# Kernel tuning notes

Measured on AMD Instinct MI355X. Metric: run time of the kernel, lower is better.

The kernel has to match this reference:

```python
import jax, jax.numpy as jnp
import numpy as np

B, T, N, D, H, C = 32, 64, 22, 512, 8, 128
DEPTH = D // H


def setup_inputs() -> dict:
    key = jax.random.key(0)
    ks = jax.random.split(key, 10)
    s = 0.02
    return {
        "x": jax.random.normal(ks[0], (B, T, N, D), jnp.float32),
        "context": jax.random.normal(ks[1], (B, C, D), jnp.float32),
        "Wq": jax.random.normal(ks[2], (N, D, D), jnp.float32) * s,  # per-joint Q proj
        "bq": jax.random.normal(ks[3], (N, D), jnp.float32) * s,
        "Wk": jax.random.normal(ks[4], (D, D), jnp.float32) * s,
        "bk": jax.random.normal(ks[5], (D,), jnp.float32) * s,
        "Wv": jax.random.normal(ks[6], (D, D), jnp.float32) * s,
        "bv": jax.random.normal(ks[7], (D,), jnp.float32) * s,
        "Wout": jax.random.normal(ks[8], (D, D), jnp.float32) * s,
        "bout": jax.random.normal(ks[9], (D,), jnp.float32) * s,
    }


def reference(x, context, Wq, bq, Wk, bk, Wv, bv, Wout, bout):
    b, t, n, d = x.shape
    c = context.shape[1]
    h, dh = H, DEPTH
    # Per-joint Q projection fused into one batched GEMM: [B,T,N,D] x [N,D,D] -> [B,T,N,D]
    q = jnp.einsum('btnd,ndf->btnf', x, Wq) + bq  # bq broadcasts over (B,T)
    # Shared K/V computed ONCE (original recomputes per joint; math identical)
    k = context @ Wk + bk  # [B,C,D]
    v = context @ Wv + bv  # [B,C,D]
    # Split heads
    qh = q.reshape(b, t, n, h, dh)
    kh = k.reshape(b, c, h, dh)
    vh = v.reshape(b, c, h, dh)
    scale = 1.0 / float(np.sqrt(dh))
    # Attention logits per joint: [B,N,H,T,C]
    logits = jnp.einsum('btnhd,bchd->bnhtc', qh, kh) * scale
    attn = jax.nn.softmax(logits, axis=-1)
    # Attend shared V, merge heads: [B,T,N,D]
    o = jnp.einsum('bnhtc,bchd->btnhd', attn, vh).reshape(b, t, n, d)
    # Shared output projection
    return o @ Wout + bout
```

## Files before the change

### kernel.cpp

```cpp
#include <hip/hip_runtime.h>
#include <hip/hip_bf16.h>

#define NB 32
#define NT 64
#define NJ 22
#define ND 512
#define NH 8
#define NC 128
#define NDH 64
#define NR 1408

typedef __attribute__((ext_vector_type(8))) short s16x8;
typedef __attribute__((ext_vector_type(4))) float fx4;

static __device__ __forceinline__ unsigned short f2bf(float f) {
    unsigned u = __builtin_bit_cast(unsigned, f);
    u += 0x7fffu + ((u >> 16) & 1u);
    return (unsigned short)(u >> 16);
}

static __device__ __forceinline__ fx4 mfma16(s16x8 a, s16x8 b, fx4 c) {
    return __builtin_amdgcn_mfma_f32_16x16x32_bf16(a, b, c, 0, 0, 0);
}

static __device__ __forceinline__ void gload16(const void* g, void* l) {
    __builtin_amdgcn_global_load_lds(
        (const __attribute__((address_space(1))) void*)g,
        (__attribute__((address_space(3))) void*)l,
        16, 0, 0);
}

template <int DIV>
__global__ __launch_bounds__(256) void convswz_k(const float* __restrict__ src,
                                                 unsigned short* __restrict__ dst)
{
    const long i = ((long)blockIdx.x * 256 + threadIdx.x) * 8;
    const unsigned row = (unsigned)(i >> 9);
    const int  key = (int)((row / (unsigned)DIV) & 7u);
    const int  c   = (int)((i >> 3) & 7);
    const int  cs  = c ^ key;
    const long j   = (i & ~63L) | ((long)cs << 3);
    const float4 a = *reinterpret_cast<const float4*>(src + i);
    const float4 b = *reinterpret_cast<const float4*>(src + i + 4);
    unsigned short t[8];
    t[0]=f2bf(a.x); t[1]=f2bf(a.y); t[2]=f2bf(a.z); t[3]=f2bf(a.w);
    t[4]=f2bf(b.x); t[5]=f2bf(b.y); t[6]=f2bf(b.z); t[7]=f2bf(b.w);
    *reinterpret_cast<s16x8*>(dst + j) = *reinterpret_cast<s16x8*>(t);
}

__global__ __launch_bounds__(256) void twconv_k(const float* __restrict__ W,
                                                unsigned short* __restrict__ Wt,
                                                long zsrc, long zdst)
{
    __shared__ float T[64][65];
    const int tid = threadIdx.x;
    W  += blockIdx.z * zsrc + (long)blockIdx.x * 64 * 512 + blockIdx.y * 64;
    Wt += blockIdx.z * zdst + (long)blockIdx.y * 64 * 512 + blockIdx.x * 64;
    const int r = tid >> 2, c0 = (tid & 3) * 16;
    #pragma unroll
    for (int i = 0; i < 4; ++i) {
        const float4 p = *reinterpret_cast<const float4*>(W + (long)r * 512 + c0 + i*4);
        T[r][c0 + i*4 + 0] = p.x; T[r][c0 + i*4 + 1] = p.y;
        T[r][c0 + i*4 + 2] = p.z; T[r][c0 + i*4 + 3] = p.w;
    }
    __syncthreads();
    unsigned short o[16];
    #pragma unroll
    for (int i = 0; i < 16; ++i) o[i] = f2bf(T[c0 + i][r]);
    const int ch0 = ((c0 >> 3) ^ (r & 7));
    *reinterpret_cast<s16x8*>(Wt + (long)r * 512 + ch0*8)       = *reinterpret_cast<s16x8*>(o);
    *reinterpret_cast<s16x8*>(Wt + (long)r * 512 + (ch0^1)*8)   = *reinterpret_cast<s16x8*>(o + 8);
}

template <typename TC, int MODE>
__global__ __launch_bounds__(256) void gemm128_k(
    const unsigned short* __restrict__ A, long lda,
    const unsigned short* __restrict__ Bt,
    const float* __restrict__ bias,
    TC* __restrict__ C, long ldc,
    long jsA, long jsW, long jsB, long jsC)
{
    __shared__ unsigned short As[2][128*64];
    __shared__ unsigned short Bs[2][128*64];

    const int tid = threadIdx.x;
    const int w = tid >> 6, lane = tid & 63;
    const long j = blockIdx.z;

    const int nx = gridDim.x;
    const int nwg = nx * gridDim.y;
    int lin = blockIdx.y * nx + blockIdx.x;
    lin = (lin & 7) * (nwg >> 3) + (lin >> 3);
    const int bx = lin % nx, by = lin / nx;

    A    += (long)bx * 128 * lda + j * jsA;
    Bt   += j * jsW + (long)by * 128 * 512;
    bias += j * jsB + by * 128;
    if constexpr (MODE == 0)
        C += (long)bx * 128 * ldc + j * jsC + by * 128;

    const int srow = lane >> 3;
    const int scol = (lane & 7) * 8;
    const unsigned short* Ag = A  + (long)(w*8 + srow) * lda + scol;
    const unsigned short* Bg = Bt + (long)(w*8 + srow) * 512 + scol;

    const int lr = lane & 15, lk = lane >> 4;
    const int wm = w >> 1, wn = w & 1;

    fx4 acc[4][4] = {};

    auto STAGE = [&](int buf, int kt) {
        char* Al = (char*)&As[buf][0] + w * 1024;
        char* Bl = (char*)&Bs[buf][0] + w * 1024;
        #pragma unroll
        for (int it = 0; it < 4; ++it)
            gload16(Ag + (long)it * 32 * lda + kt, Al + it * 4096);
        #pragma unroll
        for (int it = 0; it < 4; ++it)
            gload16(Bg + (long)it * 32 * 512 + kt, Bl + it * 4096);
    };

    auto COMPUTE = [&](int buf) {
        #pragma unroll
        for (int ks = 0; ks < 2; ++ks) {
            const int cha = (ks*4 + lk) ^ (lr & 7);
            s16x8 a[4], b[4];
            #pragma unroll
            for (int m = 0; m < 4; ++m)
                a[m] = *reinterpret_cast<const s16x8*>(&As[buf][(wm*64 + m*16 + lr)*64 + cha*8]);
            #pragma unroll
            for (int n = 0; n < 4; ++n)
                b[n] = *reinterpret_cast<const s16x8*>(&Bs[buf][(wn*64 + n*16 + lr)*64 + cha*8]);
            #pragma unroll
            for (int m = 0; m < 4; ++m)
                #pragma unroll
                for (int n = 0; n < 4; ++n)
                    acc[m][n] = mfma16(a[m], b[n], acc[m][n]);
        }
    };

    STAGE(0, 0);
    __syncthreads();
    #pragma unroll
    for (int t = 0; t < 7; ++t) {
        const int cur = t & 1;
        STAGE(cur ^ 1, (t + 1) * 64);
        COMPUTE(cur);
        __syncthreads();
    }
    COMPUTE(1);

    #pragma unroll
    for (int n = 0; n < 4; ++n) {
        const int col = wn*64 + n*16 + lr;
        const float bv = bias[col];
        #pragma unroll
        for (int m = 0; m < 4; ++m) {
            #pragma unroll
            for (int r = 0; r < 4; ++r) {
                const int row = wm*64 + m*16 + lk*4 + r;
                const float val = acc[m][n][r] + bv;
                if constexpr (MODE == 0) {
                    if constexpr (sizeof(TC) == 2)
                        reinterpret_cast<unsigned short*>(C)[(long)row*ldc + col] = f2bf(val);
                    else
                        reinterpret_cast<float*>(C)[(long)row*ldc + col] = val;
                } else {
                    const int grow = bx*128 + row;
                    const int gcol = by*128 + col;
                    const int b = grow >> 7, c = grow & 127;
                    const int hh = gcol >> 6, dh = gcol & 63;
                    unsigned short* Cp = reinterpret_cast<unsigned short*>(C);
                    if constexpr (MODE == 1) {
                        const int dhs = (dh & 7) | ((((dh >> 3) ^ (c & 7)) & 7) << 3);
                        Cp[(((long)b*8 + hh)*128 + c)*64 + dhs] = f2bf(val);
                    } else {
                        const int cs = (c & 7) | ((((c >> 3) ^ (dh & 7)) & 15) << 3);
                        Cp[(((long)b*8 + hh)*64 + dh)*128 + cs] = f2bf(val);
                    }
                }
            }
        }
    }
}

__global__ __launch_bounds__(256) void attn2_k(
    const unsigned short* __restrict__ q,
    const unsigned short* __restrict__ kt,
    const unsigned short* __restrict__ vt,
    unsigned short* __restrict__ o)
{
    __shared__ unsigned short Ps[128*136];
    __shared__ unsigned short Ks[128*64];
    __shared__ unsigned short Vs[64*128];

    const int tid = threadIdx.x;
    const int w = tid >> 6, lane = tid & 63;
    const int lr = lane & 15, lk = lane >> 4;
    const int r0 = blockIdx.x * 128;
    const int h = blockIdx.y;
    const int b = blockIdx.z;

    const unsigned short* qg = q + ((long)b*NR + r0 + w*32 + (lane>>3))*512
                                 + h*64 + (lane & 7)*8;
    const unsigned short* kg = kt + ((long)(b*8+h))*8192 + (w*4)*512 + lane*8;
    const unsigned short* vg = vt + ((long)(b*8+h))*8192 + (w*4)*512 + lane*8;

    #pragma unroll
    for (int it = 0; it < 4; ++it) {
        gload16(qg + (long)it*8*512, (char*)Ps + (w*32 + it*8)*128);
        gload16(kg + it*512, (char*)Ks + (w*4 + it)*1024);
        gload16(vg + it*512, (char*)Vs + (w*4 + it)*1024);
    }
    __syncthreads();

    s16x8 aq[2][2];
    #pragma unroll
    for (int m = 0; m < 2; ++m)
        #pragma unroll
        for (int kk = 0; kk < 2; ++kk)
            aq[m][kk] = *reinterpret_cast<const s16x8*>(
                &Ps[(w*32 + m*16 + lr)*64 + kk*32 + lk*8]);
    __syncthreads();

    fx4 s[2][8] = {};
    #pragma unroll
    for (int kk = 0; kk < 2; ++kk) {
        #pragma unroll
        for (int f = 0; f < 8; ++f) {
            const int c = f*16 + lr;
            const int chunk = (kk*4 + lk) ^ (c & 7);
            s16x8 bk = *reinterpret_cast<const s16x8*>(&Ks[c*64 + chunk*8]);
            s[0][f] = mfma16(aq[0][kk], bk, s[0][f]);
            s[1][f] = mfma16(aq[1][kk], bk, s[1][f]);
        }
    }

    const float SC = 0.125f * 1.44269504088896340736f;
    #pragma unroll
    for (int m = 0; m < 2; ++m) {
        #pragma unroll
        for (int r = 0; r < 4; ++r) {
            float mx = -3.0e38f;
            #pragma unroll
            for (int f = 0; f < 8; ++f) mx = fmaxf(mx, s[m][f][r]);
            #pragma unroll
            for (int off = 1; off < 16; off <<= 1) mx = fmaxf(mx, __shfl_xor(mx, off));
            float p[8]; float sum = 0.f;
            #pragma unroll
            for (int f = 0; f < 8; ++f) {
                p[f] = exp2f((s[m][f][r] - mx) * SC);
                sum += p[f];
            }
            #pragma unroll
            for (int off = 1; off < 16; off <<= 1) sum += __shfl_xor(sum, off);
            const float inv = 1.0f / sum;
            const int row = w*32 + m*16 + lk*4 + r;
            #pragma unroll
            for (int f = 0; f < 8; ++f)
                Ps[row*136 + f*16 + lr] = f2bf(p[f] * inv);
        }
    }

    fx4 oacc[2][4] = {};
    #pragma unroll
    for (int kt4 = 0; kt4 < 4; ++kt4) {
        s16x8 ap[2];
        #pragma unroll
        for (int m = 0; m < 2; ++m)
            ap[m] = *reinterpret_cast<const s16x8*>(
                &Ps[(w*32 + m*16 + lr)*136 + kt4*32 + lk*8]);
        #pragma unroll
        for (int bn = 0; bn < 4; ++bn) {
            const int dh = bn*16 + lr;
            const int chunk = (kt4*4 + lk) ^ (dh & 7);
            s16x8 bv = *reinterpret_cast<const s16x8*>(&Vs[dh*128 + chunk*8]);
            oacc[0][bn] = mfma16(ap[0], bv, oacc[0][bn]);
            oacc[1][bn] = mfma16(ap[1], bv, oacc[1][bn]);
        }
    }

    unsigned short* ob = o + ((long)b*NR + r0)*512 + h*64;
    #pragma unroll
    for (int m = 0; m < 2; ++m)
        #pragma unroll
        for (int bn = 0; bn < 4; ++bn)
            #pragma unroll
            for (int r = 0; r < 4; ++r) {
                const int row = w*32 + m*16 + lk*4 + r;
                const int colg = bn*16 + lr;
                const int ch = ((colg >> 3) ^ (row & 7));
                ob[(long)row*512 + ch*8 + (lr & 7)] = f2bf(oacc[m][bn][r]);
            }
}

extern "C" void kernel_launch(void* const* d_in, const int* in_sizes, int n_in,
                              void* d_out, int out_size, void* d_ws, size_t ws_size,
                              hipStream_t stream)
{
    const float* x    = (const float*)d_in[0];
    const float* ctx  = (const float*)d_in[1];
    const float* Wq   = (const float*)d_in[2];
    const float* bq   = (const float*)d_in[3];
    const float* Wk   = (const float*)d_in[4];
    const float* bk   = (const float*)d_in[5];
    const float* Wv   = (const float*)d_in[6];
    const float* bv   = (const float*)d_in[7];
    const float* Wout = (const float*)d_in[8];
    const float* bout = (const float*)d_in[9];
    float* out = (float*)d_out;

    const size_t NX  = (size_t)45056 * 512;
    const size_t NKV = (size_t)4096 * 512;
    const size_t NW  = (size_t)512 * 512;

    unsigned short* xbf   = (unsigned short*)d_ws;
    unsigned short* qbf   = xbf   + NX;
    unsigned short* cbf   = qbf   + NX;
    unsigned short* ktp   = cbf   + NKV;
    unsigned short* vtp   = ktp   + NKV;
    unsigned short* WqT   = vtp   + NKV;
    unsigned short* WkT   = WqT   + 22 * NW;
    unsigned short* WvT   = WkT   + NW;
    unsigned short* WoutT = WvT   + NW;
    unsigned short* obf   = xbf;

    convswz_k<NJ><<<dim3(NX / 2048), 256, 0, stream>>>(x, xbf);
    convswz_k<1><<<dim3(NKV / 2048), 256, 0, stream>>>(ctx, cbf);
    twconv_k<<<dim3(8, 8, 22), 256, 0, stream>>>(Wq,   WqT,   (long)NW, (long)NW);
    twconv_k<<<dim3(8, 8, 1),  256, 0, stream>>>(Wk,   WkT,   0, 0);
    twconv_k<<<dim3(8, 8, 1),  256, 0, stream>>>(Wv,   WvT,   0, 0);
    twconv_k<<<dim3(8, 8, 1),  256, 0, stream>>>(Wout, WoutT, 0, 0);

    gemm128_k<unsigned short, 0><<<dim3(16, 4, NJ), 256, 0, stream>>>(
        xbf, (long)NJ*ND, WqT, bq, qbf, (long)NJ*ND,
        (long)ND, (long)NW, (long)ND, (long)ND);

    gemm128_k<unsigned short, 1><<<dim3(32, 4, 1), 256, 0, stream>>>(
        cbf, ND, WkT, bk, ktp, ND, 0, 0, 0, 0);
    gemm128_k<unsigned short, 2><<<dim3(32, 4, 1), 256, 0, stream>>>(
        cbf, ND, WvT, bv, vtp, ND, 0, 0, 0, 0);

    attn2_k<<<dim3(NR/128, NH, NB), 256, 0, stream>>>(qbf, ktp, vtp, obf);

    gemm128_k<float, 0><<<dim3(45056/128, 4, 1), 256, 0, stream>>>(
        obf, ND, WoutT, bout, out, ND, 0, 0, 0, 0);
}
```

Baseline: 207.8 us.

## Halve attention query tile to 64 rows and alias P onto K in shared memory

The attention kernel now processes 64 query rows per block instead of 128, doubling the grid size. Shared memory shrinks from about 66KB to 40KB by reusing the K buffer for the softmax probabilities, which are stored with an XOR swizzle instead of padding. Launch bounds request 4 blocks per CU to raise occupancy and improve latency hiding. In exchange, each K/V tile is loaded from global memory twice as often across blocks, and each wave does less MFMA work per load.

After: 200.6 us. 1.04x faster.

```diff
diff --git a/kernel.cpp b/kernel.cpp
--- a/kernel.cpp
+++ b/kernel.cpp
@@ -184,46 +184,44 @@
     }
 }
 
-__global__ __launch_bounds__(256) void attn2_k(
+__global__ __launch_bounds__(256, 4) void attn3_k(
     const unsigned short* __restrict__ q,
     const unsigned short* __restrict__ kt,
     const unsigned short* __restrict__ vt,
     unsigned short* __restrict__ o)
 {
-    __shared__ unsigned short Ps[128*136];
-    __shared__ unsigned short Ks[128*64];
-    __shared__ unsigned short Vs[64*128];
+    __shared__ __align__(16) unsigned short smem[20480];
+    unsigned short* Qs = smem;
+    unsigned short* Ks = smem + 4096;
+    unsigned short* Vs = smem + 12288;
 
     const int tid = threadIdx.x;
     const int w = tid >> 6, lane = tid & 63;
     const int lr = lane & 15, lk = lane >> 4;
-    const int r0 = blockIdx.x * 128;
+    const int r0 = blockIdx.x * 64;
     const int h = blockIdx.y;
     const int b = blockIdx.z;
 
-    const unsigned short* qg = q + ((long)b*NR + r0 + w*32 + (lane>>3))*512
+    const unsigned short* qg = q + ((long)b*NR + r0 + w*16 + (lane>>3))*512
                                  + h*64 + (lane & 7)*8;
-    const unsigned short* kg = kt + ((long)(b*8+h))*8192 + (w*4)*512 + lane*8;
-    const unsigned short* vg = vt + ((long)(b*8+h))*8192 + (w*4)*512 + lane*8;
-
+    const unsigned short* kg = kt + ((long)(b*8+h))*8192 + w*2048 + lane*8;
+    const unsigned short* vg = vt + ((long)(b*8+h))*8192 + w*2048 + lane*8;
+
+    gload16(qg,            (char*)Qs + w*2048);
+    gload16(qg + 8*512,    (char*)Qs + w*2048 + 1024);
     #pragma unroll
     for (int it = 0; it < 4; ++it) {
-        gload16(qg + (long)it*8*512, (char*)Ps + (w*32 + it*8)*128);
-        gload16(kg + it*512, (char*)Ks + (w*4 + it)*1024);
-        gload16(vg + it*512, (char*)Vs + (w*4 + it)*1024);
+        gload16(kg + it*512, (char*)Ks + w*4096 + it*1024);
+        gload16(vg + it*512, (char*)Vs + w*4096 + it*1024);
     }
     __syncthreads();
 
-    s16x8 aq[2][2];
-    #pragma unroll
-    for (int m = 0; m < 2; ++m)
-        #pragma unroll
-        for (int kk = 0; kk < 2; ++kk)
-            aq[m][kk] = *reinterpret_cast<const s16x8*>(
-                &Ps[(w*32 + m*16 + lr)*64 + kk*32 + lk*8]);
-    __syncthreads();
-
-    fx4 s[2][8] = {};
+    s16x8 aq[2];
+    #pragma unroll
+    for (int kk = 0; kk < 2; ++kk)
+        aq[kk] = *reinterpret_cast<const s16x8*>(&Qs[(w*16 + lr)*64 + kk*32 + lk*8]);
+
+    fx4 s[8] = {};
     #pragma unroll
     for (int kk = 0; kk < 2; ++kk) {
         #pragma unroll
@@ -231,67 +229,63 @@
             const int c = f*16 + lr;
             const int chunk = (kk*4 + lk) ^ (c & 7);
             s16x8 bk = *reinterpret_cast<const s16x8*>(&Ks[c*64 + chunk*8]);
-            s[0][f] = mfma16(aq[0][kk], bk, s[0][f]);
-            s[1][f] = mfma16(aq[1][kk], bk, s[1][f]);
-        }
-    }
+            s[f] = mfma16(aq[kk], bk, s[f]);
+        }
+    }
+    __syncthreads();
+
+    unsigned short* P = Ks;
 
     const float SC = 0.125f * 1.44269504088896340736f;
     #pragma unroll
-    for (int m = 0; m < 2; ++m) {
-        #pragma unroll
-        for (int r = 0; r < 4; ++r) {
-            float mx = -3.0e38f;
-            #pragma unroll
-            for (int f = 0; f < 8; ++f) mx = fmaxf(mx, s[m][f][r]);
-            #pragma unroll
-            for (int off = 1; off < 16; off <<= 1) mx = fmaxf(mx, __shfl_xor(mx, off));
-            float p[8]; float sum = 0.f;
-            #pragma unroll
-            for (int f = 0; f < 8; ++f) {
-                p[f] = exp2f((s[m][f][r] - mx) * SC);
-                sum += p[f];
-            }
-            #pragma unroll
-            for (int off = 1; off < 16; off <<= 1) sum += __shfl_xor(sum, off);
-            const float inv = 1.0f / sum;
-            const int row = w*32 + m*16 + lk*4 + r;
-            #pragma unroll
-            for (int f = 0; f < 8; ++f)
-                Ps[row*136 + f*16 + lr] = f2bf(p[f] * inv);
-        }
-    }
-
-    fx4 oacc[2][4] = {};
+    for (int rr = 0; rr < 4; ++rr) {
+        const int row = w*16 + lk*4 + rr;
+        float mx = -3.0e38f;
+        #pragma unroll
+        for (int f = 0; f < 8; ++f) mx = fmaxf(mx, s[f][rr]);
+        #pragma unroll
+        for (int off = 1; off < 16; off <<= 1) mx = fmaxf(mx, __shfl_xor(mx, off));
+        float p[8]; float sum = 0.f;
+        #pragma unroll
+        for (int f = 0; f < 8; ++f) {
+            p[f] = exp2f((s[f][rr] - mx) * SC);
+            sum += p[f];
+        }
+        #pragma unroll
+        for (int off = 1; off < 16; off <<= 1) sum += __shfl_xor(sum, off);
+        const float inv = 1.0f / sum;
+        #pragma unroll
+        for (int f = 0; f < 8; ++f) {
+            const int cg = f*16 + lr;
+            P[row*128 + (((cg >> 3) ^ (row & 7)) << 3) + (cg & 7)] = f2bf(p[f] * inv);
+        }
+    }
+
+    fx4 oacc[4] = {};
     #pragma unroll
     for (int kt4 = 0; kt4 < 4; ++kt4) {
-        s16x8 ap[2];
-        #pragma unroll
-        for (int m = 0; m < 2; ++m)
-            ap[m] = *reinterpret_cast<const s16x8*>(
-                &Ps[(w*32 + m*16 + lr)*136 + kt4*32 + lk*8]);
+        const int prow = w*16 + lr;
+        s16x8 ap = *reinterpret_cast<const s16x8*>(
+            &P[prow*128 + (((kt4*4 + lk) ^ (prow & 7)) << 3)]);
         #pragma unroll
         for (int bn = 0; bn < 4; ++bn) {
             const int dh = bn*16 + lr;
             const int chunk = (kt4*4 + lk) ^ (dh & 7);
             s16x8 bv = *reinterpret_cast<const s16x8*>(&Vs[dh*128 + chunk*8]);
-            oacc[0][bn] = mfma16(ap[0], bv, oacc[0][bn]);
-            oacc[1][bn] = mfma16(ap[1], bv, oacc[1][bn]);
+            oacc[bn] = mfma16(ap, bv, oacc[bn]);
         }
     }
 
     unsigned short* ob = o + ((long)b*NR + r0)*512 + h*64;
     #pragma unroll
-    for (int m = 0; m < 2; ++m)
-        #pragma unroll
-        for (int bn = 0; bn < 4; ++bn)
-            #pragma unroll
-            for (int r = 0; r < 4; ++r) {
-                const int row = w*32 + m*16 + lk*4 + r;
-                const int colg = bn*16 + lr;
-                const int ch = ((colg >> 3) ^ (row & 7));
-                ob[(long)row*512 + ch*8 + (lr & 7)] = f2bf(oacc[m][bn][r]);
-            }
+    for (int bn = 0; bn < 4; ++bn)
+        #pragma unroll
+        for (int rr = 0; rr < 4; ++rr) {
+            const int row = w*16 + lk*4 + rr;
+            const int colg = bn*16 + lr;
+            const int ch = ((colg >> 3) ^ (row & 7));
+            ob[(long)row*512 + ch*8 + (lr & 7)] = f2bf(oacc[bn][rr]);
+        }
 }
 
 extern "C" void kernel_launch(void* const* d_in, const int* in_sizes, int n_in,
@@ -341,7 +335,7 @@
     gemm128_k<unsigned short, 2><<<dim3(32, 4, 1), 256, 0, stream>>>(
         cbf, ND, WvT, bv, vtp, ND, 0, 0, 0, 0);
 
-    attn2_k<<<dim3(NR/128, NH, NB), 256, 0, stream>>>(qbf, ktp, vtp, obf);
+    attn3_k<<<dim3(NR/64, NH, NB), 256, 0, stream>>>(qbf, ktp, vtp, obf);
 
     gemm128_k<float, 0><<<dim3(45056/128, 4, 1), 256, 0, stream>>>(
         obf, ND, WoutT, bout, out, ND, 0, 0, 0, 0);
```
